# Kernel tuning notes

Measured on AMD Instinct MI355X. Metric: run time of the kernel, lower is better.

The kernel has to match this reference:

```python
import jax, jax.numpy as jnp
import numpy as np

B, T, D, H = 2, 2048, 1024, 16
HD = D // H
DFF = 4 * D
EPS = 1e-5


def gelu_tanh(x):
    c = jnp.sqrt(2.0 / jnp.pi).astype(x.dtype)
    return 0.5 * x * (1.0 + jnp.tanh(c * (x + 0.044715 * x ** 3)))


def layernorm(x, scale, shift):
    mean = jnp.mean(x, axis=-1, keepdims=True)
    var = jnp.var(x, axis=-1, keepdims=True)  # unbiased=False
    return (x - mean) / jnp.sqrt(var + EPS) * scale + shift


def setup_inputs() -> dict:
    key = jax.random.key(0)
    ks = jax.random.split(key, 12)
    s = lambda fan_in: 1.0 / np.sqrt(fan_in)
    return {
        "x": jax.random.normal(ks[0], (B, T, D), jnp.float32),
        "wq": jax.random.normal(ks[1], (D, D), jnp.float32) * s(D),
        "wk": jax.random.normal(ks[2], (D, D), jnp.float32) * s(D),
        "wv": jax.random.normal(ks[3], (D, D), jnp.float32) * s(D),
        "wo": jax.random.normal(ks[4], (D, D), jnp.float32) * s(D),
        "bo": jnp.zeros((D,), jnp.float32),
        "ln1_scale": jnp.ones((D,), jnp.float32),
        "ln1_shift": jnp.zeros((D,), jnp.float32),
        "ln2_scale": jnp.ones((D,), jnp.float32),
        "ln2_shift": jnp.zeros((D,), jnp.float32),
        "w1": jax.random.normal(ks[5], (D, DFF), jnp.float32) * s(D),
        "b1": jnp.zeros((DFF,), jnp.float32),
        "w2": jax.random.normal(ks[6], (DFF, D), jnp.float32) * s(DFF),
        "b2": jnp.zeros((D,), jnp.float32),
    }


def reference(x, wq, wk, wv, wo, bo, ln1_scale, ln1_shift, ln2_scale, ln2_shift, w1, b1, w2, b2):
    # pre-LN attention
    h = layernorm(x, ln1_scale, ln1_shift)
    q = (h @ wq).reshape(B, T, H, HD).transpose(0, 2, 1, 3)  # [B,H,T,hd]
    k = (h @ wk).reshape(B, T, H, HD).transpose(0, 2, 1, 3)
    v = (h @ wv).reshape(B, T, H, HD).transpose(0, 2, 1, 3)
    scores = jnp.einsum('bhqd,bhkd->bhqk', q, k) / jnp.sqrt(jnp.float32(HD))
    causal = jnp.tril(jnp.ones((T, T), bool))
    scores = jnp.where(causal, scores, -jnp.inf)
    attn = jax.nn.softmax(scores, axis=-1)
    ctx = jnp.einsum('bhqk,bhkd->bhqd', attn, v)
    ctx = ctx.transpose(0, 2, 1, 3).reshape(B, T, D)
    attn_out = ctx @ wo + bo
    x = x + attn_out  # dropout p=0
    # pre-LN FFN
    h2 = layernorm(x, ln2_scale, ln2_shift)
    ff = gelu_tanh(h2 @ w1 + b1) @ w2 + b2
    return x + ff
```

## Files before the change

kernel.cpp:

```cpp
#include <hip/hip_runtime.h>
#include <hip/hip_bf16.h>
#include <stdint.h>

typedef unsigned short u16;
typedef __attribute__((ext_vector_type(8))) short s16x8;
typedef __attribute__((ext_vector_type(4))) float f32x4;

#define B_   2
#define T_   2048
#define D_   1024
#define H_   16
#define HD_  64
#define DFF_ 4096
#define M_   (B_*T_)

#define SC2F 0.18033688f

__device__ __forceinline__ u16 f2b(float f){
  uint32_t u = __float_as_uint(f);
  u += 0x7FFFu + ((u >> 16) & 1u);
  return (u16)(u >> 16);
}
__device__ __forceinline__ float b2f(u16 u){ return __uint_as_float(((uint32_t)u) << 16); }
__device__ __forceinline__ uint32_t pk2(float lo, float hi){
  uint32_t r;
  asm volatile("v_cvt_pk_bf16_f32 %0, %1, %2" : "=v"(r) : "v"(lo), "v"(hi));
  return r;
}

__device__ __forceinline__ void gl_lds16(const void* g, void* l){
  __builtin_amdgcn_global_load_lds((const __attribute__((address_space(1))) void*)g,
                                   (__attribute__((address_space(3))) void*)l, 16, 0, 0);
}

template<int N> __device__ __forceinline__ void waitvm(){
  if constexpr (N == 0)      asm volatile("s_waitcnt vmcnt(0)" ::: "memory");
  else if constexpr (N == 2) asm volatile("s_waitcnt vmcnt(2)" ::: "memory");
  else                       asm volatile("s_waitcnt vmcnt(4)" ::: "memory");
}

__global__ __launch_bounds__(256) void wconv_all(const float* __restrict__ wq,
                                                 const float* __restrict__ wk,
                                                 const float* __restrict__ wv,
                                                 const float* __restrict__ wo,
                                                 const float* __restrict__ w1,
                                                 const float* __restrict__ w2,
                                                 u16* __restrict__ wqkvT, u16* __restrict__ woT,
                                                 u16* __restrict__ w1T,   u16* __restrict__ w2T,
                                                 const float* __restrict__ x,
                                                 const float* __restrict__ ln1s,
                                                 const float* __restrict__ ln1b,
                                                 u16* __restrict__ hout){
  const int bid = blockIdx.x;
  const int tid = threadIdx.x;
  if (bid >= 3072){
    const int row = bid - 3072;
    float4 a = reinterpret_cast<const float4*>(x + ((size_t)row << 10))[tid];
    float s = a.x + a.y + a.z + a.w;
    float q = a.x*a.x + a.y*a.y + a.z*a.z + a.w*a.w;
    #pragma unroll
    for (int o = 32; o > 0; o >>= 1){ s += __shfl_xor(s, o); q += __shfl_xor(q, o); }
    __shared__ float red[8];
    const int w = tid >> 6;
    if ((tid & 63) == 0){ red[w] = s; red[4 + w] = q; }
    __syncthreads();
    float S = red[0] + red[1] + red[2] + red[3];
    float Q = red[4] + red[5] + red[6] + red[7];
    float mean = S * (1.0f/1024.0f);
    float var  = Q * (1.0f/1024.0f) - mean*mean;
    float inv = rsqrtf(var + 1e-5f);
    float4 gsc = reinterpret_cast<const float4*>(ln1s)[tid];
    float4 gsh = reinterpret_cast<const float4*>(ln1b)[tid];
    ushort4 o4;
    o4.x = f2b((a.x - mean)*inv*gsc.x + gsh.x);
    o4.y = f2b((a.y - mean)*inv*gsc.y + gsh.y);
    o4.z = f2b((a.z - mean)*inv*gsc.z + gsh.z);
    o4.w = f2b((a.w - mean)*inv*gsc.w + gsh.w);
    reinterpret_cast<ushort4*>(hout + ((size_t)row << 10))[tid] = o4;
    return;
  }
  const float* W; u16* Wt; int K, N, tk, tn;
  if (bid < 1024){
    const int which = bid >> 8, t = bid & 255; tk = t >> 4; tn = t & 15; K = 1024; N = 1024;
    W  = (which == 0) ? wq : (which == 1) ? wk : (which == 2) ? wv : wo;
    Wt = (which == 3) ? woT : wqkvT + (size_t)which * D_ * D_;
  } else if (bid < 2048){
    const int t = bid - 1024; tk = t >> 6; tn = t & 63; K = 1024; N = 4096; W = w1; Wt = w1T;
  } else {
    const int t = bid - 2048; tk = t >> 4; tn = t & 15; K = 4096; N = 1024; W = w2; Wt = w2T;
  }
  const int k0 = tk << 6, n0 = tn << 6;
  __shared__ u16 tile[64][68];
  const int rr = tid >> 4, c4 = (tid & 15) << 2;
  #pragma unroll
  for (int rep = 0; rep < 4; rep++){
    int r = rr + (rep << 4);
    float4 v = *reinterpret_cast<const float4*>(W + (size_t)(k0 + r)*N + n0 + c4);
    tile[r][c4+0] = f2b(v.x); tile[r][c4+1] = f2b(v.y);
    tile[r][c4+2] = f2b(v.z); tile[r][c4+3] = f2b(v.w);
  }
  __syncthreads();
  const int rn = tid >> 2, kb = (tid & 3) << 4;
  u16 tmp[16];
  #pragma unroll
  for (int j = 0; j < 16; j++) tmp[j] = tile[kb + j][rn];
  ushort4* dst = reinterpret_cast<ushort4*>(Wt + (size_t)(n0 + rn)*K + k0 + kb);
  dst[0] = make_ushort4(tmp[0], tmp[1], tmp[2], tmp[3]);
  dst[1] = make_ushort4(tmp[4], tmp[5], tmp[6], tmp[7]);
  dst[2] = make_ushort4(tmp[8], tmp[9], tmp[10], tmp[11]);
  dst[3] = make_ushort4(tmp[12], tmp[13], tmp[14], tmp[15]);
}

__global__ __launch_bounds__(256) void vtrans(const u16* __restrict__ Vs, u16* __restrict__ Vt){
  const int bh = blockIdx.y, tt = blockIdx.x;
  __shared__ u16 tile[64][68];
  const int tid = threadIdx.x;
  const u16* src = Vs + ((size_t)bh*T_ + tt*64)*HD_;
  const int rr = tid >> 4, c4 = (tid & 15) << 2;
  #pragma unroll
  for (int rep = 0; rep < 4; rep++){
    int r = rr + (rep << 4);
    ushort4 v = *reinterpret_cast<const ushort4*>(src + (size_t)r*HD_ + c4);
    tile[r][c4+0] = v.x; tile[r][c4+1] = v.y; tile[r][c4+2] = v.z; tile[r][c4+3] = v.w;
  }
  __syncthreads();
  const int rn = tid >> 2, kb = (tid & 3) << 4;
  u16 tmp[16];
  #pragma unroll
  for (int j = 0; j < 16; j++) tmp[j] = tile[kb + j][rn];
  ushort4* dst = reinterpret_cast<ushort4*>(Vt + ((size_t)bh*HD_ + rn)*T_ + tt*64 + kb);
  dst[0] = make_ushort4(tmp[0], tmp[1], tmp[2], tmp[3]);
  dst[1] = make_ushort4(tmp[4], tmp[5], tmp[6], tmp[7]);
  dst[2] = make_ushort4(tmp[8], tmp[9], tmp[10], tmp[11]);
  dst[3] = make_ushort4(tmp[12], tmp[13], tmp[14], tmp[15]);
}

__global__ __launch_bounds__(256) void reduce2(const u16* __restrict__ p,
                                               const float* __restrict__ bias,
                                               const float* __restrict__ resid,
                                               float* __restrict__ out){
  const size_t idx = ((size_t)blockIdx.x << 8) + threadIdx.x;
  ushort4 a4 = reinterpret_cast<const ushort4*>(p)[idx];
  ushort4 b4 = reinterpret_cast<const ushort4*>(p)[idx + (((size_t)M_*D_) >> 2)];
  float4 r = reinterpret_cast<const float4*>(resid)[idx];
  float4 bb = reinterpret_cast<const float4*>(bias)[threadIdx.x];
  float4 o;
  o.x = b2f(a4.x) + b2f(b4.x) + r.x + bb.x;
  o.y = b2f(a4.y) + b2f(b4.y) + r.y + bb.y;
  o.z = b2f(a4.z) + b2f(b4.z) + r.z + bb.z;
  o.w = b2f(a4.w) + b2f(b4.w) + r.w + bb.w;
  reinterpret_cast<float4*>(out)[idx] = o;
}

__global__ __launch_bounds__(256) void reduce_ln(const u16* __restrict__ p,
                                                 const float* __restrict__ bias,
                                                 const float* __restrict__ resid,
                                                 const float* __restrict__ sc,
                                                 const float* __restrict__ sh,
                                                 float* __restrict__ x1,
                                                 u16* __restrict__ h2){
  const int row = blockIdx.x;
  const int tid = threadIdx.x;
  const size_t idx = ((size_t)row << 8) + tid;
  ushort4 a4 = reinterpret_cast<const ushort4*>(p)[idx];
  ushort4 b4 = reinterpret_cast<const ushort4*>(p)[idx + (((size_t)M_*D_) >> 2)];
  float4 r  = reinterpret_cast<const float4*>(resid)[idx];
  float4 bb = reinterpret_cast<const float4*>(bias)[tid];
  float4 v;
  v.x = b2f(a4.x) + b2f(b4.x) + r.x + bb.x;
  v.y = b2f(a4.y) + b2f(b4.y) + r.y + bb.y;
  v.z = b2f(a4.z) + b2f(b4.z) + r.z + bb.z;
  v.w = b2f(a4.w) + b2f(b4.w) + r.w + bb.w;
  reinterpret_cast<float4*>(x1)[idx] = v;
  float s = v.x + v.y + v.z + v.w;
  float q = v.x*v.x + v.y*v.y + v.z*v.z + v.w*v.w;
  #pragma unroll
  for (int o = 32; o > 0; o >>= 1){ s += __shfl_xor(s, o); q += __shfl_xor(q, o); }
  __shared__ float red[8];
  const int w = tid >> 6;
  if ((tid & 63) == 0){ red[w] = s; red[4 + w] = q; }
  __syncthreads();
  float S = red[0] + red[1] + red[2] + red[3];
  float Q = red[4] + red[5] + red[6] + red[7];
  float mean = S * (1.0f/1024.0f);
  float var  = Q * (1.0f/1024.0f) - mean*mean;
  float inv = rsqrtf(var + 1e-5f);
  float4 gsc = reinterpret_cast<const float4*>(sc)[tid];
  float4 gsh = reinterpret_cast<const float4*>(sh)[tid];
  ushort4 o4;
  o4.x = f2b((v.x - mean)*inv*gsc.x + gsh.x);
  o4.y = f2b((v.y - mean)*inv*gsc.y + gsh.y);
  o4.z = f2b((v.z - mean)*inv*gsc.z + gsh.z);
  o4.w = f2b((v.w - mean)*inv*gsc.w + gsh.w);
  reinterpret_cast<ushort4*>(h2 + ((size_t)row << 10))[tid] = o4;
}

template<int EPI, int NF>
__global__ __launch_bounds__(512, 2) void gemm8(const u16* __restrict__ A, const u16* __restrict__ Bt,
                                                const float* __restrict__ bias,
                                                void* __restrict__ Cv, int M, int N, int K, int lda){
  constexpr int BROWS = NF * 32;
  __shared__ __align__(16) u16 LA[2][2][128*64];
  __shared__ __align__(16) u16 LB[2][2][BROWS*64];
  const int tid = threadIdx.x;
  const int lane = tid & 63;
  const int w = tid >> 6;
  const int wm = w >> 2, wn = w & 3;
  const int g = lane >> 4, l15 = lane & 15;
  const int bnb = (wn & 1) * (NF * 16);

  const int nx = gridDim.x, ny = gridDim.y;
  const int nwg = nx * ny * gridDim.z;
  const int flat = blockIdx.x + nx * (blockIdx.y + ny * blockIdx.z);
  const int nfid = (flat & 7) * (nwg >> 3) + (flat >> 3);
  const int tn = nfid % nx;
  const int rest = nfid / nx;
  const int tm = rest % ny;
  const int kz = rest / ny;
  const int tn0 = tn * (NF * 64);
  const int tm0 = tm << 8;
  const u16* Az = A  + (size_t)kz * K;
  const u16* Bz = Bt + (size_t)kz * K;

  const int arow0 = tid >> 3,         asl0 = (((tid) & 7) ^ (arow0 & 7)) << 3;
  const int arow1 = (tid + 512) >> 3, asl1 = (((tid + 512) & 7) ^ (arow1 & 7)) << 3;

  f32x4 acc[8][NF];
  #pragma unroll
  for (int i = 0; i < 8; i++)
    #pragma unroll
    for (int j = 0; j < NF; j++) acc[i][j] = (f32x4){0.f,0.f,0.f,0.f};
  s16x8 bf[NF][2];

#define STG_A(db, h, tt) do{                                                        \
    gl_lds16(Az + (size_t)(tm0 + (h)*128 + arow0)*lda + ((tt) << 6) + asl0,         \
             &LA[db][h][tid*8]);                                                    \
    gl_lds16(Az + (size_t)(tm0 + (h)*128 + arow1)*lda + ((tt) << 6) + asl1,         \
             &LA[db][h][(tid + 512)*8]);                                            \
  }while(0)
#define STG_B(db, h, tt) do{                                                        \
    gl_lds16(Bz + (size_t)(tn0 + (h)*BROWS + arow0)*lda + ((tt) << 6) + asl0,       \
             &LB[db][h][tid*8]);                                                    \
    if constexpr (NF == 4){                                                         \
      gl_lds16(Bz + (size_t)(tn0 + (h)*BROWS + arow1)*lda + ((tt) << 6) + asl1,     \
               &LB[db][h][(tid + 512)*8]);                                          \
    }                                                                               \
  }while(0)
#define LDAF(db, mf, kk) (*reinterpret_cast<const s16x8*>(                          \
    &LA[db][wm][((mf)*16 + l15)*64 + ((((kk)*4 + g) ^ (l15 & 7)) << 3)]))
#define LDBF(db, nf, kk) (*reinterpret_cast<const s16x8*>(                          \
    &LB[db][wn >> 1][(bnb + (nf)*16 + l15)*64 + ((((kk)*4 + g) ^ (l15 & 7)) << 3)]))
#define BLOAD(db) do{ _Pragma("unroll")                                             \
    for (int nf = 0; nf < NF; nf++){ bf[nf][0] = LDBF(db, nf, 0);                   \
                                     bf[nf][1] = LDBF(db, nf, 1); } }while(0)
#define PH(db, MFA, MFB, STG, WV) do{                                               \
    s16x8 a00 = LDAF(db, MFA, 0), a01 = LDAF(db, MFA, 1);                           \
    s16x8 a10 = LDAF(db, MFB, 0), a11 = LDAF(db, MFB, 1);                           \
    STG;                                                                            \
    WV;                                                                             \
    __builtin_amdgcn_s_barrier();                                                   \
    __builtin_amdgcn_s_setprio(1);                                                  \
    _Pragma("unroll")                                                               \
    for (int nf = 0; nf < NF; nf++){                                                \
      acc[MFA][nf] = __builtin_amdgcn_mfma_f32_16x16x32_bf16(a00, bf[nf][0], acc[MFA][nf], 0,0,0); \
      acc[MFA][nf] = __builtin_amdgcn_mfma_f32_16x16x32_bf16(a01, bf[nf][1], acc[MFA][nf], 0,0,0); \
      acc[MFB][nf] = __builtin_amdgcn_mfma_f32_16x16x32_bf16(a10, bf[nf][0], acc[MFB][nf], 0,0,0); \
      acc[MFB][nf] = __builtin_amdgcn_mfma_f32_16x16x32_bf16(a11, bf[nf][1], acc[MFB][nf], 0,0,0); \
    }                                                                               \
    __builtin_amdgcn_s_setprio(0);                                                  \
    __builtin_amdgcn_s_barrier();                                                   \
  }while(0)

  const int NT = K >> 6;
  STG_B(0, 0, 0); STG_B(0, 1, 0); STG_A(0, 0, 0); STG_A(0, 1, 0);
  STG_B(1, 0, 1); STG_B(1, 1, 1);
  waitvm<NF>();
  __builtin_amdgcn_s_barrier();

  for (int t = 0; t < NT; t += 2){
    const bool last = (t + 2 >= NT);
    BLOAD(0);
    PH(0, 0, 1, STG_A(1, 0, t + 1), );
    PH(0, 2, 3, STG_A(1, 1, t + 1), );
    PH(0, 4, 5, if (!last) STG_B(0, 0, t + 2), );
    PH(0, 6, 7, if (!last) STG_B(0, 1, t + 2),
                if (last) waitvm<0>(); else waitvm<NF>(););
    BLOAD(1);
    PH(1, 0, 1, if (!last) STG_A(0, 0, t + 2), );
    PH(1, 2, 3, if (!last) STG_A(0, 1, t + 2), );
    PH(1, 4, 5, if (!last) STG_B(1, 0, t + 3), );
    PH(1, 6, 7, if (!last) STG_B(1, 1, t + 3),
                if (last) waitvm<0>(); else waitvm<NF>(););
  }
#undef STG_A
#undef STG_B
#undef LDAF
#undef LDBF
#undef BLOAD
#undef PH

  #pragma unroll
  for (int mf = 0; mf < 8; mf++){
    const int mb = tm0 + wm*128 + mf*16 + (g << 2);
    #pragma unroll
    for (int nf = 0; nf < NF; nf++){
      const int n = tn0 + wn*(NF*16) + nf*16 + l15;
      #pragma unroll
      for (int rr = 0; rr < 4; rr++){
        const int m = mb + rr;
        float v = acc[mf][nf][rr];
        if constexpr (EPI == 0){
          ((u16*)Cv)[(size_t)kz*((size_t)M*N) + (size_t)m*N + n] = f2b(v);
        } else if constexpr (EPI == 1){
          const int sel = n >> 10, nn = n & 1023;
          const int hh = nn >> 6, d = nn & 63;
          if (sel == 0) v *= SC2F;
          ((u16*)Cv)[(size_t)sel*((size_t)M_*D_) +
                     ((((size_t)(m >> 11)*H_ + hh)*T_ + (m & 2047)) << 6) + d] = f2b(v);
        } else {
          float u = v + bias[n];
          float t2 = 0.7978845608f*(u + 0.044715f*u*u*u);
          float e = __expf(2.0f*t2);
          float th = 1.0f - 2.0f/(e + 1.0f);
          ((u16*)Cv)[(size_t)m*N + n] = f2b(0.5f*u*(1.0f + th));
        }
      }
    }
  }
}

__global__ __launch_bounds__(256) void attn_k(const u16* __restrict__ Qg, const u16* __restrict__ Kg,
                                              const u16* __restrict__ Vg, u16* __restrict__ ctx){
  const int flat = blockIdx.x + (blockIdx.y << 4);
  const int xcd = flat & 7, j_ = flat >> 3;
  const int bh  = ((j_ & 3) << 3) + xcd;
  const int pr_ = j_ >> 2;
  const int tid = threadIdx.x;
  const int lane = tid & 63;
  const int w = tid >> 6;
  const int g = lane >> 4, l15 = lane & 15;

  __shared__ __align__(16) u16 Qs[64*64];
  __shared__ __align__(16) u16 Ks[2][64*64];
  __shared__ __align__(16) u16 Vt[2][64*64];
  __shared__ __align__(16) u16 Pl[4][16*64];

  const size_t hb = (size_t)bh * ((size_t)T_*HD_);
  const u16* Qh = Qg + hb;
  const u16* Kh = Kg + hb;
  const u16* Vh = Vg + hb;
  const int b = bh >> 4, hh = bh & 15;

  const int s_r0 = tid >> 3,        s_c0 = (((tid & 7) ^ (s_r0 & 7)) << 3);
  const int s_r1 = (256+tid) >> 3,  s_c1 = ((((256+tid) & 7) ^ (s_r1 & 7)) << 3);

  for (int ph = 0; ph < 2; ++ph){
    const int qt = ph ? (31 - pr_) : pr_;

    gl_lds16(Qh + (size_t)(qt*64 + s_r0)*HD_ + s_c0, Qs + tid*8);
    gl_lds16(Qh + (size_t)(qt*64 + s_r1)*HD_ + s_c1, Qs + (256+tid)*8);
    gl_lds16(Kh + (size_t)(s_r0)*HD_ + s_c0, Ks[0] + tid*8);
    gl_lds16(Kh + (size_t)(s_r1)*HD_ + s_c1, Ks[0] + (256+tid)*8);
    gl_lds16(Vh + (size_t)s_r0*T_ + s_c0, Vt[0] + tid*8);
    gl_lds16(Vh + (size_t)s_r1*T_ + s_c1, Vt[0] + (256+tid)*8);
    __syncthreads();

    s16x8 qa[2];
    #pragma unroll
    for (int kk = 0; kk < 2; kk++){
      int ra = (w << 4) + l15;
      int slot = (kk << 2) + g;
      qa[kk] = *reinterpret_cast<const s16x8*>(Qs + ra*64 + ((slot ^ (ra & 7)) << 3));
    }

    f32x4 accO[4];
    #pragma unroll
    for (int j = 0; j < 4; j++) accO[j] = (f32x4){0.f,0.f,0.f,0.f};
    float mrow = -1e30f, lrow = 0.f;
    const int qlt = (w << 4) + l15;

    for (int kt = 0; kt <= qt; ++kt){
      const int cur = kt & 1, nxt = cur ^ 1;
      const bool pf = (kt < qt);

      if (pf){
        gl_lds16(Kh + (size_t)((kt+1)*64 + s_r0)*HD_ + s_c0, Ks[nxt] + tid*8);
        gl_lds16(Kh + (size_t)((kt+1)*64 + s_r1)*HD_ + s_c1, Ks[nxt] + (256+tid)*8);
        gl_lds16(Vh + (size_t)s_r0*T_ + (kt+1)*64 + s_c0, Vt[nxt] + tid*8);
        gl_lds16(Vh + (size_t)s_r1*T_ + (kt+1)*64 + s_c1, Vt[nxt] + (256+tid)*8);
      }

      f32x4 accS[4];
      #pragma unroll
      for (int j = 0; j < 4; j++) accS[j] = (f32x4){0.f,0.f,0.f,0.f};
      __builtin_amdgcn_s_setprio(1);
      #pragma unroll
      for (int jn = 0; jn < 4; jn++){
        #pragma unroll
        for (int kk = 0; kk < 2; kk++){
          int rb = (jn << 4) + l15;
          int slot = (kk << 2) + g;
          s16x8 kf = *reinterpret_cast<const s16x8*>(Ks[cur] + rb*64 + ((slot ^ (rb & 7)) << 3));
          accS[jn] = __builtin_amdgcn_mfma_f32_16x16x32_bf16(kf, qa[kk], accS[jn], 0, 0, 0);
        }
      }
      __builtin_amdgcn_s_setprio(0);

      float sv[4][4];
      #pragma unroll
      for (int jn = 0; jn < 4; jn++)
        #pragma unroll
        for (int rr = 0; rr < 4; rr++){
          float xv = accS[jn][rr];
          if (kt == qt){
            int kl = (jn << 4) + (g << 2) + rr;
            if (kl > qlt) xv = -1e30f;
          }
          sv[jn][rr] = xv;
        }

      float rmax = sv[0][0];
      #pragma unroll
      for (int jn = 0; jn < 4; jn++)
        #pragma unroll
        for (int rr = 0; rr < 4; rr++) rmax = fmaxf(rmax, sv[jn][rr]);
      rmax = fmaxf(rmax, __shfl_xor(rmax, 16));
      rmax = fmaxf(rmax, __shfl_xor(rmax, 32));

      if (__any(rmax > mrow + 8.0f)){
        float mn = fmaxf(mrow, rmax);
        float sf = exp2f(mrow - mn);
        mrow = mn;
        lrow *= sf;
        #pragma unroll
        for (int rr = 0; rr < 4; rr++){
          float sfr = __shfl(sf, ((lane >> 4) << 2) + rr);
          #pragma unroll
          for (int jn = 0; jn < 4; jn++) accO[jn][rr] *= sfr;
        }
      }

      float tsum = 0.f;
      #pragma unroll
      for (int jn = 0; jn < 4; jn++){
        float pv0 = exp2f(sv[jn][0] - mrow);
        float pv1 = exp2f(sv[jn][1] - mrow);
        float pv2 = exp2f(sv[jn][2] - mrow);
        float pv3 = exp2f(sv[jn][3] - mrow);
        tsum += (pv0 + pv1) + (pv2 + pv3);
        int slot = (jn << 1) | (g >> 1);
        int base = l15*64 + (((slot ^ (l15 & 7)) & 7) << 3) + ((g & 1) << 2);
        uint2 pkd = make_uint2(pk2(pv0, pv1), pk2(pv2, pv3));
        *reinterpret_cast<uint2*>(&Pl[w][base]) = pkd;
      }
      tsum += __shfl_xor(tsum, 16);
      tsum += __shfl_xor(tsum, 32);
      lrow += tsum;

      __builtin_amdgcn_s_setprio(1);
      #pragma unroll
      for (int kk = 0; kk < 2; kk++){
        int slot = (kk << 2) + g;
        s16x8 pa = *reinterpret_cast<const s16x8*>(
            &Pl[w][l15*64 + (((slot ^ (l15 & 7)) & 7) << 3)]);
        #pragma unroll
        for (int jn = 0; jn < 4; jn++){
          int vd = (jn << 4) + l15;
          s16x8 vbf = *reinterpret_cast<const s16x8*>(
              Vt[cur] + vd*64 + (((slot ^ (vd & 7)) & 7) << 3));
          accO[jn] = __builtin_amdgcn_mfma_f32_16x16x32_bf16(pa, vbf, accO[jn], 0, 0, 0);
        }
      }
      __builtin_amdgcn_s_setprio(0);

      __syncthreads();
    }

    #pragma unroll
    for (int rr = 0; rr < 4; rr++){
      float lr = __shfl(lrow, ((lane >> 4) << 2) + rr);
      float inv = 1.0f / lr;
      int qrow = qt*64 + (w << 4) + (g << 2) + rr;
      size_t rowbase = ((size_t)(b*T_ + qrow) << 10) + ((size_t)hh << 6);
      #pragma unroll
      for (int jn = 0; jn < 4; jn++){
        int d = (jn << 4) + l15;
        ctx[rowbase + d] = f2b(accO[jn][rr] * inv);
      }
    }
  }
}

extern "C" void kernel_launch(void* const* d_in, const int* in_sizes, int n_in,
                              void* d_out, int out_size, void* d_ws, size_t ws_size,
                              hipStream_t stream){
  (void)in_sizes; (void)n_in; (void)out_size; (void)ws_size;
  const float* x    = (const float*)d_in[0];
  const float* wq   = (const float*)d_in[1];
  const float* wk   = (const float*)d_in[2];
  const float* wv   = (const float*)d_in[3];
  const float* wo   = (const float*)d_in[4];
  const float* bo   = (const float*)d_in[5];
  const float* ln1s = (const float*)d_in[6];
  const float* ln1b = (const float*)d_in[7];
  const float* ln2s = (const float*)d_in[8];
  const float* ln2b = (const float*)d_in[9];
  const float* w1   = (const float*)d_in[10];
  const float* b1   = (const float*)d_in[11];
  const float* w2   = (const float*)d_in[12];
  const float* b2   = (const float*)d_in[13];
  float* out = (float*)d_out;

  char* p = (char*)d_ws;
  u16*  wqkvT = (u16*)p;  p += (size_t)3*D_*D_*2;
  u16*  woT   = (u16*)p;  p += (size_t)D_*D_*2;
  u16*  w1T   = (u16*)p;  p += (size_t)D_*DFF_*2;
  u16*  w2T   = (u16*)p;  p += (size_t)DFF_*D_*2;
  u16*  h     = (u16*)p;  p += (size_t)M_*D_*2;
  u16*  qb    = (u16*)p;  p += (size_t)M_*D_*2;
  u16*  kb    = (u16*)p;  p += (size_t)M_*D_*2;
  u16*  vb    = (u16*)p;  p += (size_t)M_*D_*2;
  u16*  ctx   = (u16*)p;  p += (size_t)M_*D_*2;
  float* x1   = (float*)p; p += (size_t)M_*D_*4;
  u16*  h2    = (u16*)p;  p += (size_t)M_*D_*2;
  u16*  ff1   = (u16*)p;  p += (size_t)M_*DFF_*2;
  (void)kb;
  u16* part = h;

  dim3 blk(256), blk8(512);
  wconv_all<<<3072 + M_, blk, 0, stream>>>(wq, wk, wv, wo, w1, w2, wqkvT, woT, w1T, w2T,
                                           x, ln1s, ln1b, h);
  gemm8<1,4><<<dim3(12,16,1), blk8, 0, stream>>>(h, wqkvT, nullptr, qb, M_, 3*D_, D_, D_);
  vtrans<<<dim3(32,32), blk, 0, stream>>>(vb, h);
  attn_k<<<dim3(16,32), blk, 0, stream>>>(qb, qb + (size_t)M_*D_, h, ctx);
  gemm8<0,2><<<dim3(8,16,2), blk8, 0, stream>>>(ctx, woT, nullptr, part, M_, D_, D_/2, D_);
  reduce_ln<<<M_, blk, 0, stream>>>(part, bo, x, ln2s, ln2b, x1, h2);
  gemm8<3,4><<<dim3(16,16,1), blk8, 0, stream>>>(h2, w1T, b1, ff1, M_, DFF_, D_, D_);
  gemm8<0,2><<<dim3(8,16,2), blk8, 0, stream>>>(ff1, w2T, nullptr, part, M_, D_, DFF_/2, DFF_);
  reduce2<<<M_, blk, 0, stream>>>(part, b2, x1, out);
}
```

Measured before the change: 231.6 us.

## Use 128-row query tiles with 512-thread attention blocks and retune QKV GEMM grid

The attention kernel now processes 128 query rows per block with 8 waves instead of 64 rows with 4 waves. Each K/V tile loaded into shared memory is reused by twice as many query rows, which halves K/V global traffic per query and the number of blocks. Causal masking is now applied on the last two key tiles using global indices. The QKV GEMM launch also changes its template parameter and doubles the grid in x, trading tile shape for more blocks. The risk is fewer blocks (256) and more load imbalance across the causal diagonal.

Result: slower. 237.3 us (+2.5%).

```diff
diff --git a/kernel.cpp b/kernel.cpp
--- a/kernel.cpp
+++ b/kernel.cpp
@@ -329,21 +329,20 @@
   }
 }
 
-__global__ __launch_bounds__(256) void attn_k(const u16* __restrict__ Qg, const u16* __restrict__ Kg,
+__global__ __launch_bounds__(512) void attn_k(const u16* __restrict__ Qg, const u16* __restrict__ Kg,
                                               const u16* __restrict__ Vg, u16* __restrict__ ctx){
-  const int flat = blockIdx.x + (blockIdx.y << 4);
-  const int xcd = flat & 7, j_ = flat >> 3;
-  const int bh  = ((j_ & 3) << 3) + xcd;
-  const int pr_ = j_ >> 2;
+  const int flat = blockIdx.x + (blockIdx.y << 3);
+  const int xcd = flat & 7, j_ = (flat >> 3) & 3, pr_ = flat >> 5;
+  const int bh  = (j_ << 3) + xcd;
   const int tid = threadIdx.x;
   const int lane = tid & 63;
   const int w = tid >> 6;
   const int g = lane >> 4, l15 = lane & 15;
 
-  __shared__ __align__(16) u16 Qs[64*64];
+  __shared__ __align__(16) u16 Qs[128*64];
   __shared__ __align__(16) u16 Ks[2][64*64];
   __shared__ __align__(16) u16 Vt[2][64*64];
-  __shared__ __align__(16) u16 Pl[4][16*64];
+  __shared__ __align__(16) u16 Pl[8][16*64];
 
   const size_t hb = (size_t)bh * ((size_t)T_*HD_);
   const u16* Qh = Qg + hb;
@@ -351,18 +350,17 @@
   const u16* Vh = Vg + hb;
   const int b = bh >> 4, hh = bh & 15;
 
-  const int s_r0 = tid >> 3,        s_c0 = (((tid & 7) ^ (s_r0 & 7)) << 3);
-  const int s_r1 = (256+tid) >> 3,  s_c1 = ((((256+tid) & 7) ^ (s_r1 & 7)) << 3);
+  const int s_r0 = tid >> 3,         s_c0 = (((tid & 7) ^ (s_r0 & 7)) << 3);
+  const int s_r1 = (tid + 512) >> 3, s_c1 = ((((tid + 512) & 7) ^ (s_r1 & 7)) << 3);
 
   for (int ph = 0; ph < 2; ++ph){
-    const int qt = ph ? (31 - pr_) : pr_;
-
-    gl_lds16(Qh + (size_t)(qt*64 + s_r0)*HD_ + s_c0, Qs + tid*8);
-    gl_lds16(Qh + (size_t)(qt*64 + s_r1)*HD_ + s_c1, Qs + (256+tid)*8);
-    gl_lds16(Kh + (size_t)(s_r0)*HD_ + s_c0, Ks[0] + tid*8);
-    gl_lds16(Kh + (size_t)(s_r1)*HD_ + s_c1, Ks[0] + (256+tid)*8);
+    const int qt = ph ? (15 - pr_) : pr_;
+    const int NKT = (qt << 1) + 2;
+
+    gl_lds16(Qh + (size_t)(qt*128 + s_r0)*HD_ + s_c0, Qs + tid*8);
+    gl_lds16(Qh + (size_t)(qt*128 + s_r1)*HD_ + s_c1, Qs + (tid+512)*8);
+    gl_lds16(Kh + (size_t)s_r0*HD_ + s_c0, Ks[0] + tid*8);
     gl_lds16(Vh + (size_t)s_r0*T_ + s_c0, Vt[0] + tid*8);
-    gl_lds16(Vh + (size_t)s_r1*T_ + s_c1, Vt[0] + (256+tid)*8);
     __syncthreads();
 
     s16x8 qa[2];
@@ -377,17 +375,15 @@
     #pragma unroll
     for (int j = 0; j < 4; j++) accO[j] = (f32x4){0.f,0.f,0.f,0.f};
     float mrow = -1e30f, lrow = 0.f;
-    const int qlt = (w << 4) + l15;
-
-    for (int kt = 0; kt <= qt; ++kt){
+    const int qgl = qt*128 + (w << 4) + l15;
+
+    for (int kt = 0; kt < NKT; ++kt){
       const int cur = kt & 1, nxt = cur ^ 1;
-      const bool pf = (kt < qt);
+      const bool pf = (kt + 1 < NKT);
 
       if (pf){
         gl_lds16(Kh + (size_t)((kt+1)*64 + s_r0)*HD_ + s_c0, Ks[nxt] + tid*8);
-        gl_lds16(Kh + (size_t)((kt+1)*64 + s_r1)*HD_ + s_c1, Ks[nxt] + (256+tid)*8);
         gl_lds16(Vh + (size_t)s_r0*T_ + (kt+1)*64 + s_c0, Vt[nxt] + tid*8);
-        gl_lds16(Vh + (size_t)s_r1*T_ + (kt+1)*64 + s_c1, Vt[nxt] + (256+tid)*8);
       }
 
       f32x4 accS[4];
@@ -406,24 +402,21 @@
       }
       __builtin_amdgcn_s_setprio(0);
 
-      float sv[4][4];
+      if (kt >= (qt << 1)){
+        #pragma unroll
+        for (int jn = 0; jn < 4; jn++)
+          #pragma unroll
+          for (int rr = 0; rr < 4; rr++){
+            int kgl = kt*64 + (jn << 4) + (g << 2) + rr;
+            if (kgl > qgl) accS[jn][rr] = -1e30f;
+          }
+      }
+
+      float rmax = accS[0][0];
       #pragma unroll
       for (int jn = 0; jn < 4; jn++)
         #pragma unroll
-        for (int rr = 0; rr < 4; rr++){
-          float xv = accS[jn][rr];
-          if (kt == qt){
-            int kl = (jn << 4) + (g << 2) + rr;
-            if (kl > qlt) xv = -1e30f;
-          }
-          sv[jn][rr] = xv;
-        }
-
-      float rmax = sv[0][0];
-      #pragma unroll
-      for (int jn = 0; jn < 4; jn++)
-        #pragma unroll
-        for (int rr = 0; rr < 4; rr++) rmax = fmaxf(rmax, sv[jn][rr]);
+        for (int rr = 0; rr < 4; rr++) rmax = fmaxf(rmax, accS[jn][rr]);
       rmax = fmaxf(rmax, __shfl_xor(rmax, 16));
       rmax = fmaxf(rmax, __shfl_xor(rmax, 32));
 
@@ -443,10 +436,10 @@
       float tsum = 0.f;
       #pragma unroll
       for (int jn = 0; jn < 4; jn++){
-        float pv0 = exp2f(sv[jn][0] - mrow);
-        float pv1 = exp2f(sv[jn][1] - mrow);
-        float pv2 = exp2f(sv[jn][2] - mrow);
-        float pv3 = exp2f(sv[jn][3] - mrow);
+        float pv0 = exp2f(accS[jn][0] - mrow);
+        float pv1 = exp2f(accS[jn][1] - mrow);
+        float pv2 = exp2f(accS[jn][2] - mrow);
+        float pv3 = exp2f(accS[jn][3] - mrow);
         tsum += (pv0 + pv1) + (pv2 + pv3);
         int slot = (jn << 1) | (g >> 1);
         int base = l15*64 + (((slot ^ (l15 & 7)) & 7) << 3) + ((g & 1) << 2);
@@ -480,7 +473,7 @@
     for (int rr = 0; rr < 4; rr++){
       float lr = __shfl(lrow, ((lane >> 4) << 2) + rr);
       float inv = 1.0f / lr;
-      int qrow = qt*64 + (w << 4) + (g << 2) + rr;
+      int qrow = qt*128 + (w << 4) + (g << 2) + rr;
       size_t rowbase = ((size_t)(b*T_ + qrow) << 10) + ((size_t)hh << 6);
       #pragma unroll
       for (int jn = 0; jn < 4; jn++){
@@ -530,9 +523,9 @@
   dim3 blk(256), blk8(512);
   wconv_all<<<3072 + M_, blk, 0, stream>>>(wq, wk, wv, wo, w1, w2, wqkvT, woT, w1T, w2T,
                                            x, ln1s, ln1b, h);
-  gemm8<1,4><<<dim3(12,16,1), blk8, 0, stream>>>(h, wqkvT, nullptr, qb, M_, 3*D_, D_, D_);
+  gemm8<1,2><<<dim3(24,16,1), blk8, 0, stream>>>(h, wqkvT, nullptr, qb, M_, 3*D_, D_, D_);
   vtrans<<<dim3(32,32), blk, 0, stream>>>(vb, h);
-  attn_k<<<dim3(16,32), blk, 0, stream>>>(qb, qb + (size_t)M_*D_, h, ctx);
+  attn_k<<<dim3(8,32), blk8, 0, stream>>>(qb, qb + (size_t)M_*D_, h, ctx);
   gemm8<0,2><<<dim3(8,16,2), blk8, 0, stream>>>(ctx, woT, nullptr, part, M_, D_, D_/2, D_);
   reduce_ln<<<M_, blk, 0, stream>>>(part, bo, x, ln2s, ln2b, x1, h2);
   gemm8<3,4><<<dim3(16,16,1), blk8, 0, stream>>>(h2, w1T, b1, ff1, M_, DFF_, D_, D_);
```
